# Optimization experiments

Measured on AMD Instinct MI355X. Metric: run time of the kernel, lower is better.

Reference implementation:

```python
import jax, jax.numpy as jnp
import numpy as np

B = 16384
S = 7
CELL = 1.0 / 7.0   # CELL_SILE
LC = 5.0           # lambda_coord
LN = 0.5           # lambda_noobj


def setup_inputs() -> dict:
    key = jax.random.key(0)
    k1, k2, k3 = jax.random.split(key, 3)
    predictions = jax.random.normal(k1, (B, S, S, 30), dtype=jnp.float32)
    targets = jax.random.uniform(k2, (B, S, S, 30), dtype=jnp.float32)
    # channel 4 is the objectness flag; code requires it to be exactly 0 or 1
    conf = (jax.random.uniform(k3, (B, S, S)) < 0.25).astype(jnp.float32)
    targets = targets.at[..., 4].set(conf)
    return {"predictions": predictions, "targets": targets}


def _box_corners(xy, wh):
    # Faithful to the original in-place bug: x2y2 uses the ALREADY-UPDATED x1y1
    xy1 = xy * CELL - wh * 0.5
    xy2 = xy1 * CELL + wh * 0.5
    return xy1, xy2


def _loss_terms(predictions, targets):
    p = predictions.reshape(-1, 30)   # [N, 30], N = B*S*S
    t = targets.reshape(-1, 30)
    obj = (t[:, 4] == 1.0).astype(p.dtype)
    noobj = (t[:, 4] == 0.0).astype(p.dtype)

    # no-object confidence loss on cols 4 and 9
    noobj_loss = LN * jnp.sum(noobj * (jnp.square(p[:, 4] - t[:, 4]) + jnp.square(p[:, 9] - t[:, 9])))

    # two predicted boxes per cell: cols 0:4 and 5:9 ; wh are sqrt-encoded -> square
    pb = jnp.stack([p[:, 0:4], p[:, 5:9]], axis=1)        # [N, 2, 4]
    pxy1, pxy2 = _box_corners(pb[..., 0:2], jnp.square(pb[..., 2:4]))  # [N,2,2]
    txy1, txy2 = _box_corners(t[:, None, 0:2], jnp.square(t[:, None, 2:4]))  # [N,1,2]

    # torchvision.ops.box_iou math (no clamp on areas, clamp(0) on intersection)
    lt = jnp.maximum(pxy1, txy1)
    rb = jnp.minimum(pxy2, txy2)
    inter = jnp.prod(jnp.clip(rb - lt, 0.0, None), axis=-1)   # [N, 2]
    area_p = jnp.prod(pxy2 - pxy1, axis=-1)                   # [N, 2]
    area_t = jnp.prod(txy2 - txy1, axis=-1)                   # [N, 1]
    iou = inter / (area_p + area_t - inter)                   # [N, 2]

    idx = jnp.argmax(iou, axis=1)                             # responsible box in {0,1}

    cols = idx[:, None] * 5 + jnp.arange(4)[None, :]          # [N, 4]
    cp = jnp.take_along_axis(p, cols, axis=1)
    ct = jnp.take_along_axis(t, cols, axis=1)
    center_loss = LC * jnp.sum(obj * jnp.sum(jnp.square(cp[:, 0:2] - ct[:, 0:2]), axis=1))
    wh_loss = LC * jnp.sum(obj * jnp.sum(jnp.square(cp[:, 2:4] - ct[:, 2:4]), axis=1))

    ccol = (idx * 5 + 4)[:, None]
    conf_loss = LC * jnp.sum(obj * jnp.square(jnp.take_along_axis(p, ccol, axis=1) - jnp.take_along_axis(t, ccol, axis=1))[:, 0])

    kcol = (jnp.argmax(t[:, 10:30], axis=1) + 10)[:, None]
    cls_loss = LC * jnp.sum(obj * jnp.square(jnp.take_along_axis(p, kcol, axis=1) - jnp.take_along_axis(t, kcol, axis=1))[:, 0])

    total = noobj_loss + center_loss + wh_loss + conf_loss + cls_loss
    return cls_loss, conf_loss, center_loss + wh_loss, total


def reference(predictions, targets):
    return _loss_terms(predictions, targets)
```

## Files before the change

kernel.cpp:

```cpp
#include <hip/hip_runtime.h>


constexpr int   WSZ  = 64;
constexpr int   NC   = 16384 * 7 * 7;
constexpr int   NT   = NC / WSZ;
constexpr int   GRID = 4096;
constexpr float CELL = 1.0f / 7.0f;
constexpr float LC   = 5.0f;
constexpr float LN   = 0.5f;

__launch_bounds__(WSZ, 4)
__global__ void yolo_partial(const float* __restrict__ P, const float* __restrict__ T,
                             float4* __restrict__ ws)
{
    __shared__ float sT[WSZ * 30];
    const int lane = threadIdx.x;
    float a_cls = 0.f, a_conf = 0.f, a_cw = 0.f, a_noobj = 0.f;

    for (int tile = blockIdx.x; tile < NT; tile += GRID) {
        const size_t base = (size_t)tile * (WSZ * 30);

        const float4* gT = reinterpret_cast<const float4*>(T + base);
        float4* s4 = reinterpret_cast<float4*>(sT);
        #pragma unroll
        for (int k = 0; k < 8; ++k) {
            int idx = k * WSZ + lane;
            if (idx < 480) s4[idx] = gT[idx];
        }

        const float* prow = P + base + (size_t)lane * 30;
        float pv[10];
        #pragma unroll
        for (int j = 0; j < 5; ++j) {
            float2 v = reinterpret_cast<const float2*>(prow)[j];
            pv[2 * j] = v.x; pv[2 * j + 1] = v.y;
        }
        __syncthreads();

        const float* tt = sT + lane * 30;
        float tv[30];
        #pragma unroll
        for (int j = 0; j < 15; ++j) {
            float2 v = reinterpret_cast<const float2*>(tt)[j];
            tv[2 * j] = v.x; tv[2 * j + 1] = v.y;
        }

        int kc = 10;
        float best = tv[10];
        #pragma unroll
        for (int k = 11; k < 30; ++k) {
            if (tv[k] > best) { best = tv[k]; kc = k; }
        }
        float2 pg = *reinterpret_cast<const float2*>(prow + (kc & ~1));
        float pk = (kc & 1) ? pg.y : pg.x;

        const float t4 = tv[4];
        const float obj   = (t4 == 1.0f) ? 1.0f : 0.0f;
        const float noobj = (t4 == 0.0f) ? 1.0f : 0.0f;

        float d4 = pv[4] - t4;
        float d9 = pv[9] - tv[9];
        a_noobj += noobj * (d4 * d4 + d9 * d9);

        float tw2 = tv[2] * tv[2], th2 = tv[3] * tv[3];
        float tx1 = tv[0] * CELL - 0.5f * tw2;
        float tx2 = tx1 * CELL + 0.5f * tw2;
        float ty1 = tv[1] * CELL - 0.5f * th2;
        float ty2 = ty1 * CELL + 0.5f * th2;
        float area_t = (tx2 - tx1) * (ty2 - ty1);

        float iou0, iou1;
        #pragma unroll
        for (int b = 0; b < 2; ++b) {
            float bw2 = pv[5 * b + 2] * pv[5 * b + 2];
            float bh2 = pv[5 * b + 3] * pv[5 * b + 3];
            float px1 = pv[5 * b + 0] * CELL - 0.5f * bw2;
            float px2 = px1 * CELL + 0.5f * bw2;
            float py1 = pv[5 * b + 1] * CELL - 0.5f * bh2;
            float py2 = py1 * CELL + 0.5f * bh2;
            float ltx = fmaxf(px1, tx1), lty = fmaxf(py1, ty1);
            float rbx = fminf(px2, tx2), rby = fminf(py2, ty2);
            float inter = fmaxf(rbx - ltx, 0.0f) * fmaxf(rby - lty, 0.0f);
            float area_p = (px2 - px1) * (py2 - py1);
            float iou = inter / (area_p + area_t - inter);
            if (b == 0) iou0 = iou; else iou1 = iou;
        }
        const bool b1 = (iou1 > iou0);

        float cpx = b1 ? pv[5] : pv[0], ctx = b1 ? tv[5] : tv[0];
        float cpy = b1 ? pv[6] : pv[1], cty = b1 ? tv[6] : tv[1];
        float cpw = b1 ? pv[7] : pv[2], ctw = b1 ? tv[7] : tv[2];
        float cph = b1 ? pv[8] : pv[3], cth = b1 ? tv[8] : tv[3];
        float cpc = b1 ? pv[9] : pv[4], ctc = b1 ? tv[9] : tv[4];

        float dx = cpx - ctx, dy = cpy - cty;
        float dw = cpw - ctw, dh = cph - cth;
        a_cw   += obj * (dx * dx + dy * dy + dw * dw + dh * dh);
        float dc = cpc - ctc;
        a_conf += obj * dc * dc;
        float dk = pk - best;
        a_cls  += obj * dk * dk;

        __syncthreads();
    }

    float vals[4] = { a_cls, a_conf, a_cw, a_noobj };
    #pragma unroll
    for (int c = 0; c < 4; ++c) {
        #pragma unroll
        for (int off = 32; off > 0; off >>= 1)
            vals[c] += __shfl_down(vals[c], off, 64);
    }
    if (lane == 0)
        ws[blockIdx.x] = make_float4(vals[0], vals[1], vals[2], vals[3]);
}

__launch_bounds__(1024, 1)
__global__ void yolo_reduce(const float4* __restrict__ ws, float* __restrict__ out)
{
    __shared__ float red[4][16];
    const int tid = threadIdx.x;

    float s0 = 0.f, s1 = 0.f, s2 = 0.f, s3 = 0.f;
    for (int b = tid; b < GRID; b += 1024) {
        float4 v = ws[b];
        s0 += v.x; s1 += v.y; s2 += v.z; s3 += v.w;
    }
    float vals[4] = { s0, s1, s2, s3 };
    #pragma unroll
    for (int c = 0; c < 4; ++c) {
        #pragma unroll
        for (int off = 32; off > 0; off >>= 1)
            vals[c] += __shfl_down(vals[c], off, 64);
        if ((tid & 63) == 0) red[c][tid >> 6] = vals[c];
    }
    __syncthreads();
    if (tid == 0) {
        float t0 = 0.f, t1 = 0.f, t2 = 0.f, t3 = 0.f;
        #pragma unroll
        for (int w = 0; w < 16; ++w) {
            t0 += red[0][w]; t1 += red[1][w]; t2 += red[2][w]; t3 += red[3][w];
        }
        out[0] = LC * t0;
        out[1] = LC * t1;
        out[2] = LC * t2;
        out[3] = LN * t3 + LC * (t0 + t1 + t2);
    }
}

extern "C" void kernel_launch(void* const* d_in, const int* in_sizes, int n_in,
                              void* d_out, int out_size, void* d_ws, size_t ws_size,
                              hipStream_t stream) {
    const float* P = (const float*)d_in[0];
    const float* T = (const float*)d_in[1];
    float* out = (float*)d_out;
    float4* ws = (float4*)d_ws;

    yolo_partial<<<GRID, WSZ, 0, stream>>>(P, T, ws);
    yolo_reduce<<<1, 1024, 0, stream>>>(ws, out);
}
```

Before: 208.3 us.

## Map one thread per cell with direct global loads, dropping LDS staging

Replaces the grid-stride loop over 64-cell tiles, which staged targets through shared memory, with a flat launch of 256-thread blocks where each thread handles one cell and loads its target row straight from global memory with strided float2 loads. A per-block cross-wave shared-memory reduction replaces the per-wave partial write, so GRID grows to NC/256 (3136) partials. This removes the LDS round trip and the per-iteration barriers and raises occupancy. The cost is uncoalesced 120-byte-strided global loads for targets, which lean on the cache to merge accesses.

```diff
diff --git a/kernel.cpp b/kernel.cpp
--- a/kernel.cpp
+++ b/kernel.cpp
@@ -1,108 +1,90 @@
 #include <hip/hip_runtime.h>
 
 
-constexpr int   WSZ  = 64;
+constexpr int   BLK  = 256;
 constexpr int   NC   = 16384 * 7 * 7;
-constexpr int   NT   = NC / WSZ;
-constexpr int   GRID = 4096;
+constexpr int   GRID = NC / BLK;
 constexpr float CELL = 1.0f / 7.0f;
 constexpr float LC   = 5.0f;
 constexpr float LN   = 0.5f;
 
-__launch_bounds__(WSZ, 4)
+__launch_bounds__(BLK, 8)
 __global__ void yolo_partial(const float* __restrict__ P, const float* __restrict__ T,
                              float4* __restrict__ ws)
 {
-    __shared__ float sT[WSZ * 30];
-    const int lane = threadIdx.x;
-    float a_cls = 0.f, a_conf = 0.f, a_cw = 0.f, a_noobj = 0.f;
+    const int tid  = threadIdx.x;
+    const int cell = blockIdx.x * BLK + tid;
+    const float* trow = T + (size_t)cell * 30;
+    const float* prow = P + (size_t)cell * 30;
 
-    for (int tile = blockIdx.x; tile < NT; tile += GRID) {
-        const size_t base = (size_t)tile * (WSZ * 30);
+    float tv[30];
+    #pragma unroll
+    for (int j = 0; j < 15; ++j) {
+        float2 v = reinterpret_cast<const float2*>(trow)[j];
+        tv[2 * j] = v.x; tv[2 * j + 1] = v.y;
+    }
+    float pv[10];
+    #pragma unroll
+    for (int j = 0; j < 5; ++j) {
+        float2 v = reinterpret_cast<const float2*>(prow)[j];
+        pv[2 * j] = v.x; pv[2 * j + 1] = v.y;
+    }
 
-        const float4* gT = reinterpret_cast<const float4*>(T + base);
-        float4* s4 = reinterpret_cast<float4*>(sT);
-        #pragma unroll
-        for (int k = 0; k < 8; ++k) {
-            int idx = k * WSZ + lane;
-            if (idx < 480) s4[idx] = gT[idx];
-        }
+    int kc = 10;
+    float best = tv[10];
+    #pragma unroll
+    for (int k = 11; k < 30; ++k) {
+        if (tv[k] > best) { best = tv[k]; kc = k; }
+    }
+    float2 pg = *reinterpret_cast<const float2*>(prow + (kc & ~1));
+    float pk = (kc & 1) ? pg.y : pg.x;
 
-        const float* prow = P + base + (size_t)lane * 30;
-        float pv[10];
-        #pragma unroll
-        for (int j = 0; j < 5; ++j) {
-            float2 v = reinterpret_cast<const float2*>(prow)[j];
-            pv[2 * j] = v.x; pv[2 * j + 1] = v.y;
-        }
-        __syncthreads();
+    const float t4 = tv[4];
+    const float obj   = (t4 == 1.0f) ? 1.0f : 0.0f;
+    const float noobj = (t4 == 0.0f) ? 1.0f : 0.0f;
 
-        const float* tt = sT + lane * 30;
-        float tv[30];
-        #pragma unroll
-        for (int j = 0; j < 15; ++j) {
-            float2 v = reinterpret_cast<const float2*>(tt)[j];
-            tv[2 * j] = v.x; tv[2 * j + 1] = v.y;
-        }
+    float d4 = pv[4] - t4;
+    float d9 = pv[9] - tv[9];
+    float a_noobj = noobj * (d4 * d4 + d9 * d9);
 
-        int kc = 10;
-        float best = tv[10];
-        #pragma unroll
-        for (int k = 11; k < 30; ++k) {
-            if (tv[k] > best) { best = tv[k]; kc = k; }
-        }
-        float2 pg = *reinterpret_cast<const float2*>(prow + (kc & ~1));
-        float pk = (kc & 1) ? pg.y : pg.x;
+    float tw2 = tv[2] * tv[2], th2 = tv[3] * tv[3];
+    float tx1 = tv[0] * CELL - 0.5f * tw2;
+    float tx2 = tx1 * CELL + 0.5f * tw2;
+    float ty1 = tv[1] * CELL - 0.5f * th2;
+    float ty2 = ty1 * CELL + 0.5f * th2;
+    float area_t = (tx2 - tx1) * (ty2 - ty1);
 
-        const float t4 = tv[4];
-        const float obj   = (t4 == 1.0f) ? 1.0f : 0.0f;
-        const float noobj = (t4 == 0.0f) ? 1.0f : 0.0f;
+    float iou0, iou1;
+    #pragma unroll
+    for (int b = 0; b < 2; ++b) {
+        float bw2 = pv[5 * b + 2] * pv[5 * b + 2];
+        float bh2 = pv[5 * b + 3] * pv[5 * b + 3];
+        float px1 = pv[5 * b + 0] * CELL - 0.5f * bw2;
+        float px2 = px1 * CELL + 0.5f * bw2;
+        float py1 = pv[5 * b + 1] * CELL - 0.5f * bh2;
+        float py2 = py1 * CELL + 0.5f * bh2;
+        float ltx = fmaxf(px1, tx1), lty = fmaxf(py1, ty1);
+        float rbx = fminf(px2, tx2), rby = fminf(py2, ty2);
+        float inter = fmaxf(rbx - ltx, 0.0f) * fmaxf(rby - lty, 0.0f);
+        float area_p = (px2 - px1) * (py2 - py1);
+        float iou = inter / (area_p + area_t - inter);
+        if (b == 0) iou0 = iou; else iou1 = iou;
+    }
+    const bool b1 = (iou1 > iou0);
 
-        float d4 = pv[4] - t4;
-        float d9 = pv[9] - tv[9];
-        a_noobj += noobj * (d4 * d4 + d9 * d9);
+    float cpx = b1 ? pv[5] : pv[0], ctx = b1 ? tv[5] : tv[0];
+    float cpy = b1 ? pv[6] : pv[1], cty = b1 ? tv[6] : tv[1];
+    float cpw = b1 ? pv[7] : pv[2], ctw = b1 ? tv[7] : tv[2];
+    float cph = b1 ? pv[8] : pv[3], cth = b1 ? tv[8] : tv[3];
+    float cpc = b1 ? pv[9] : pv[4], ctc = b1 ? tv[9] : tv[4];
 
-        float tw2 = tv[2] * tv[2], th2 = tv[3] * tv[3];
-        float tx1 = tv[0] * CELL - 0.5f * tw2;
-        float tx2 = tx1 * CELL + 0.5f * tw2;
-        float ty1 = tv[1] * CELL - 0.5f * th2;
-        float ty2 = ty1 * CELL + 0.5f * th2;
-        float area_t = (tx2 - tx1) * (ty2 - ty1);
-
-        float iou0, iou1;
-        #pragma unroll
-        for (int b = 0; b < 2; ++b) {
-            float bw2 = pv[5 * b + 2] * pv[5 * b + 2];
-            float bh2 = pv[5 * b + 3] * pv[5 * b + 3];
-            float px1 = pv[5 * b + 0] * CELL - 0.5f * bw2;
-            float px2 = px1 * CELL + 0.5f * bw2;
-            float py1 = pv[5 * b + 1] * CELL - 0.5f * bh2;
-            float py2 = py1 * CELL + 0.5f * bh2;
-            float ltx = fmaxf(px1, tx1), lty = fmaxf(py1, ty1);
-            float rbx = fminf(px2, tx2), rby = fminf(py2, ty2);
-            float inter = fmaxf(rbx - ltx, 0.0f) * fmaxf(rby - lty, 0.0f);
-            float area_p = (px2 - px1) * (py2 - py1);
-            float iou = inter / (area_p + area_t - inter);
-            if (b == 0) iou0 = iou; else iou1 = iou;
-        }
-        const bool b1 = (iou1 > iou0);
-
-        float cpx = b1 ? pv[5] : pv[0], ctx = b1 ? tv[5] : tv[0];
-        float cpy = b1 ? pv[6] : pv[1], cty = b1 ? tv[6] : tv[1];
-        float cpw = b1 ? pv[7] : pv[2], ctw = b1 ? tv[7] : tv[2];
-        float cph = b1 ? pv[8] : pv[3], cth = b1 ? tv[8] : tv[3];
-        float cpc = b1 ? pv[9] : pv[4], ctc = b1 ? tv[9] : tv[4];
-
-        float dx = cpx - ctx, dy = cpy - cty;
-        float dw = cpw - ctw, dh = cph - cth;
-        a_cw   += obj * (dx * dx + dy * dy + dw * dw + dh * dh);
-        float dc = cpc - ctc;
-        a_conf += obj * dc * dc;
-        float dk = pk - best;
-        a_cls  += obj * dk * dk;
-
-        __syncthreads();
-    }
+    float dx = cpx - ctx, dy = cpy - cty;
+    float dw = cpw - ctw, dh = cph - cth;
+    float a_cw   = obj * (dx * dx + dy * dy + dw * dw + dh * dh);
+    float dc = cpc - ctc;
+    float a_conf = obj * dc * dc;
+    float dk = pk - best;
+    float a_cls  = obj * dk * dk;
 
     float vals[4] = { a_cls, a_conf, a_cw, a_noobj };
     #pragma unroll
@@ -111,8 +93,20 @@
         for (int off = 32; off > 0; off >>= 1)
             vals[c] += __shfl_down(vals[c], off, 64);
     }
-    if (lane == 0)
-        ws[blockIdx.x] = make_float4(vals[0], vals[1], vals[2], vals[3]);
+    __shared__ float red[4][4];
+    const int wave = tid >> 6;
+    if ((tid & 63) == 0) {
+        red[0][wave] = vals[0]; red[1][wave] = vals[1];
+        red[2][wave] = vals[2]; red[3][wave] = vals[3];
+    }
+    __syncthreads();
+    if (tid == 0) {
+        ws[blockIdx.x] = make_float4(
+            red[0][0] + red[0][1] + red[0][2] + red[0][3],
+            red[1][0] + red[1][1] + red[1][2] + red[1][3],
+            red[2][0] + red[2][1] + red[2][2] + red[2][3],
+            red[3][0] + red[3][1] + red[3][2] + red[3][3]);
+    }
 }
 
 __launch_bounds__(1024, 1)
@@ -156,6 +150,6 @@
     float* out = (float*)d_out;
     float4* ws = (float4*)d_ws;
 
-    yolo_partial<<<GRID, WSZ, 0, stream>>>(P, T, ws);
+    yolo_partial<<<GRID, BLK, 0, stream>>>(P, T, ws);
     yolo_reduce<<<1, 1024, 0, stream>>>(ws, out);
 }
```

After: 207.2 us. About the same (-0.6%).
